# Performance work log

Measured on AMD Instinct MI355X. Metric: run time of the kernel, lower is better.

The kernel has to match this reference:

```python
import jax, jax.numpy as jnp
import numpy as np
from jax import lax

FEAT_STRIDE = 16
NMS_THRESH = 0.7
N_PRE = 6000   # test-mode n_test_pre_nms
N_POST = 300   # test-mode n_test_post_nms
MIN_SIZE = 16.0
SCALE = 1.0
RATIOS = (0.5, 1.0, 2.0)
ANCHOR_SCALES = (8, 16, 32)
BASE = 16
N_ANCHOR = len(RATIOS) * len(ANCHOR_SCALES)  # 9


def _anchor_base():
    py = px = BASE / 2.0
    ab = np.zeros((N_ANCHOR, 4), np.float32)
    for i, r in enumerate(RATIOS):
        for j, s in enumerate(ANCHOR_SCALES):
            h = BASE * s * np.sqrt(r)
            w = BASE * s * np.sqrt(1.0 / r)
            k = i * len(ANCHOR_SCALES) + j
            ab[k] = [py - h / 2.0, px - w / 2.0, py + h / 2.0, px + w / 2.0]
    return ab


def _anchors(hh, ww):
    # enumerate_shifted_anchor: (y1,x1,y2,x2) anchors for every feature cell
    ab = _anchor_base()
    sy = np.arange(0, hh * FEAT_STRIDE, FEAT_STRIDE)
    sx = np.arange(0, ww * FEAT_STRIDE, FEAT_STRIDE)
    SX, SY = np.meshgrid(sx, sy)
    shift = np.stack([SY.ravel(), SX.ravel(), SY.ravel(), SX.ravel()], 1)
    anc = (ab[None, :, :] + shift[:, None, :]).reshape(-1, 4).astype(np.float32)
    return jnp.asarray(anc)


def _iou(b):
    # b: [N,4] (y1,x1,y2,x2) -> [N,N] IoU
    y1, x1, y2, x2 = b[:, 0], b[:, 1], b[:, 2], b[:, 3]
    area = (y2 - y1) * (x2 - x1)
    ih = jnp.clip(jnp.minimum(y2[:, None], y2[None, :]) - jnp.maximum(y1[:, None], y1[None, :]), 0.0)
    iw = jnp.clip(jnp.minimum(x2[:, None], x2[None, :]) - jnp.maximum(x1[:, None], x1[None, :]), 0.0)
    inter = ih * iw
    return inter / (area[:, None] + area[None, :] - inter + 1e-9)


def _propose(loc, fg, anchor, img_h, img_w):
    # loc:[M,4] fg:[M] anchor:[M,4]  -> padded [N_POST,4] rois + valid mask
    ah = anchor[:, 2] - anchor[:, 0]
    aw = anchor[:, 3] - anchor[:, 1]
    acy = anchor[:, 0] + 0.5 * ah
    acx = anchor[:, 1] + 0.5 * aw
    cy = loc[:, 0] * ah + acy
    cx = loc[:, 1] * aw + acx
    h = jnp.exp(loc[:, 2]) * ah
    w = jnp.exp(loc[:, 3]) * aw
    roi = jnp.stack([
        jnp.clip(cy - 0.5 * h, 0.0, img_h),
        jnp.clip(cx - 0.5 * w, 0.0, img_w),
        jnp.clip(cy + 0.5 * h, 0.0, img_h),
        jnp.clip(cx + 0.5 * w, 0.0, img_w),
    ], axis=1)
    hs = roi[:, 2] - roi[:, 0]
    ws = roi[:, 3] - roi[:, 1]
    ms = MIN_SIZE * SCALE
    valid = (hs >= ms) & (ws >= ms)
    sc = jnp.where(valid, fg, -jnp.inf)  # drop too-small boxes from ranking
    top_sc, idx = lax.top_k(sc, N_PRE)   # score-sorted pre-NMS candidates
    boxes = roi[idx]
    ok = lax.stop_gradient(jnp.isfinite(top_sc))
    sup = lax.stop_gradient(_iou(boxes) > NMS_THRESH)  # [N_PRE,N_PRE]
    tri = jnp.arange(N_PRE)

    def body(i, keep):
        suppressed = jnp.any(keep & sup[:, i] & (tri < i))
        return keep.at[i].set(ok[i] & ~suppressed)

    keep = lax.fori_loop(0, N_PRE, body, jnp.zeros((N_PRE,), bool))
    rank = jnp.cumsum(keep.astype(jnp.int32)) - 1
    sel = keep & (rank < N_POST)
    tgt = jnp.where(sel, rank, N_POST)  # N_POST is out-of-bounds -> dropped
    out = jnp.zeros((N_POST, 4), boxes.dtype).at[tgt].set(boxes, mode='drop')
    vmask = jnp.zeros((N_POST,), bool).at[tgt].set(True, mode='drop')
    return out, vmask


def reference(x, conv1_w, conv1_b, score_w, score_b, loc_w, loc_b, img_h, img_w):
    n, _, hh, ww = x.shape
    anchor = _anchors(hh, ww)
    h = jax.nn.relu(
        lax.conv_general_dilated(x, conv1_w, (1, 1), 'SAME',
                                 dimension_numbers=('NCHW', 'OIHW', 'NCHW'))
        + conv1_b[None, :, None, None])
    locs = jnp.einsum('nchw,oc->nohw', h, loc_w[:, :, 0, 0]) + loc_b[None, :, None, None]
    scr = jnp.einsum('nchw,oc->nohw', h, score_w[:, :, 0, 0]) + score_b[None, :, None, None]
    rpn_locs = locs.transpose(0, 2, 3, 1).reshape(n, -1, 4)          # [n,M,4]
    scr_t = scr.transpose(0, 2, 3, 1)                                 # [n,hh,ww,2A]
    soft = jax.nn.softmax(scr_t.reshape(n, hh, ww, N_ANCHOR, 2), axis=-1)
    fg = soft[..., 1].reshape(n, -1)                                  # [n,M]
    rpn_scores = scr_t.reshape(n, -1, 2)
    rois, vmask = jax.vmap(lambda l, f: _propose(l, f, anchor, img_h, img_w))(rpn_locs, fg)
    roi_indices = jnp.broadcast_to(jnp.arange(n, dtype=jnp.int32)[:, None], (n, N_POST))
    return rpn_locs, rpn_scores, rois, roi_indices, anchor, vmask


def setup_inputs() -> dict:
    key = jax.random.key(0)
    ks = jax.random.split(key, 4)
    x = jax.random.normal(ks[0], (2, 512, 64, 64), jnp.float32)
    conv1_w = 0.01 * jax.random.normal(ks[1], (512, 512, 3, 3), jnp.float32)
    conv1_b = jnp.zeros((512,), jnp.float32)
    score_w = 0.01 * jax.random.normal(ks[2], (N_ANCHOR * 2, 512, 1, 1), jnp.float32)
    score_b = jnp.zeros((N_ANCHOR * 2,), jnp.float32)
    loc_w = 0.01 * jax.random.normal(ks[3], (N_ANCHOR * 4, 512, 1, 1), jnp.float32)
    loc_b = jnp.zeros((N_ANCHOR * 4,), jnp.float32)
    return {"x": x, "conv1_w": conv1_w, "conv1_b": conv1_b,
            "score_w": score_w, "score_b": score_b,
            "loc_w": loc_w, "loc_b": loc_b,
            "img_h": 1024, "img_w": 1024}
```

## Files before the change

kernel.cpp:

```cpp
#include <hip/hip_runtime.h>
#include <hip/hip_bf16.h>
#include <math.h>
#include <cstdint>

typedef unsigned long long u64;
typedef unsigned int u32;
typedef _Float16 half8 __attribute__((ext_vector_type(8)));
typedef float floatx4 __attribute__((ext_vector_type(4)));

#define NANCH 36864
#define SEG 65536
#define N_PRE 6000
#define N_POST 300
#define NW 96
#define NPADC 6144

#define O0 0
#define O1 294912
#define O2 442368
#define O3 444768
#define O4 445368
#define O5 592824

#define WS_XHI   0
#define WS_XLO   2097152
#define WS_WHI   4194304
#define WS_WLO   5373952
#define WS_WSLT  6553600
#define WS_WSLB  6586368
#define WS_H     6586432
#define WS_GUARD 10780736
#define WS_FG    0
#define WS_ROI   73728
#define WS_KEYS  368640
#define WS_SBOX  630784
#define WS_ALIVE 679936
#define WS_MASK  4194304

#define HSCALE 9.5367431640625e-07f

__device__ __forceinline__ void gl_lds16(const void* g, void* l) {
  __builtin_amdgcn_global_load_lds(
      (const __attribute__((address_space(1))) u32*)g,
      (__attribute__((address_space(3))) u32*)l, 16, 0, 0);
}

__device__ __forceinline__ u64 bcast64(u64 v, int src) {
  u32 lo = (u32)__shfl((int)(v & 0xFFFFFFFFull), src);
  u32 hi = (u32)__shfl((int)(v >> 32), src);
  return ((u64)hi << 32) | lo;
}

__global__ __launch_bounds__(256) void prep_all(
    const float* __restrict__ x, const float* __restrict__ w,
    const float* __restrict__ lw, const float* __restrict__ sw,
    const float* __restrict__ lb, const float* __restrict__ sb,
    float4* __restrict__ h, float4* __restrict__ guard,
    _Float16* __restrict__ xhi, _Float16* __restrict__ xlo,
    _Float16* __restrict__ whi, _Float16* __restrict__ wlo,
    float* __restrict__ wslt, float* __restrict__ wslb) {
  __shared__ float s[64 * 65];
  const int b = blockIdx.x, tid = threadIdx.x;
  if (b < 4097) {
    int idx = b * 256 + tid;
    if (idx < 1048576) h[idx] = make_float4(0.f, 0.f, 0.f, 0.f);
    else if (idx < 1048576 + 16) guard[idx - 1048576] = make_float4(0.f, 0.f, 0.f, 0.f);
    return;
  }
  if (b < 5121) {
    int l = b - 4097;
    int pt = l & 63, cg = (l >> 6) & 7, n = l >> 9;
    const int c0 = cg << 6, p0 = pt << 6;
#pragma unroll
    for (int kk = 0; kk < 16; ++kk) {
      int e = tid + (kk << 8);
      int ci = e >> 6, pi = e & 63;
      s[ci * 65 + pi] = x[(((size_t)(n * 512 + c0 + ci)) << 12) + p0 + pi];
    }
    __syncthreads();
#pragma unroll
    for (int kk = 0; kk < 16; ++kk) {
      int e = tid + (kk << 8);
      int ci = e & 63, pi = e >> 6;
      float sv = s[ci * 65 + pi] * 1024.f;
      _Float16 hi = (_Float16)sv;
      _Float16 lo = (_Float16)(sv - (float)hi);
      size_t off = (((size_t)(n << 12) + p0 + pi) << 9) + c0 + ci;
      xhi[off] = hi;
      xlo[off] = lo;
    }
    return;
  }
  if (b < 5697) {
    int l = b - 5121;
    int ct = l & 7, ot = (l >> 3) & 7, t = l >> 6;
    const int c0 = ct << 6, o0 = ot << 6;
#pragma unroll
    for (int kk = 0; kk < 16; ++kk) {
      int e = tid + (kk << 8);
      int ci = e & 63, oi = e >> 6;
      float sv = w[(size_t)(o0 + oi) * 4608 + (c0 + ci) * 9 + t] * 1024.f;
      _Float16 hi = (_Float16)sv;
      _Float16 lo = (_Float16)(sv - (float)hi);
      size_t off = ((size_t)((t << 9) + o0 + oi) << 9) + c0 + ci;
      whi[off] = hi;
      wlo[off] = lo;
    }
    return;
  }
  {
    int e = (b - 5697) * 256 + tid;
    if (e < 32768) {
      int c = e >> 6, o = e & 63;
      float v = 0.f;
      if (o < 36) v = lw[o * 512 + c];
      else if (o < 54) v = sw[(o - 36) * 512 + c];
      wslt[e] = v;
    } else if (e < 32832) {
      int o = e - 32768;
      float v = 0.f;
      if (o < 36) v = lb[o];
      else if (o < 54) v = sb[o - 36];
      wslb[o] = v;
    }
  }
}

__global__ __launch_bounds__(256) void conv_mfma(
    const _Float16* __restrict__ xhi, const _Float16* __restrict__ xlo,
    const _Float16* __restrict__ whi, const _Float16* __restrict__ wlo,
    const float* __restrict__ guard, float* __restrict__ hout) {
  __shared__ _Float16 aHi[4 * 68 * 32];
  __shared__ _Float16 aLo[4 * 68 * 32];
  __shared__ _Float16 bHi[128 * 32];
  __shared__ _Float16 bLo[128 * 32];
  const int tid = threadIdx.x;
  const int lane = tid & 63, w = tid >> 6;
  const int ptile = blockIdx.x;
  const int og = blockIdx.y;
  const int kq = blockIdx.z;
  const int n = ptile >> 5;
  const int y0 = (ptile & 31) << 1;
  const int o0 = og << 7;
  const int l15 = lane & 15, l16 = lane >> 4;
  const int ry = w >> 1;
  const int wo = (w & 1) << 6;

  floatx4 acc[4][4];
#pragma unroll
  for (int a = 0; a < 4; ++a)
#pragma unroll
    for (int b = 0; b < 4; ++b) acc[a][b] = (floatx4)0.f;

  for (int s = 0; s < 8; ++s) {
    const int c0 = (kq << 8) + (s << 5);
    __syncthreads();
    for (int i = w; i < 17; i += 4) {
      int chunk = (i << 6) + lane;
      int p = chunk >> 2, q = chunk & 3;
      int r = p / 68, xs = p - r * 68;
      int y = y0 - 1 + r, xg = xs - 1;
      bool ok = ((unsigned)y < 64u) && ((unsigned)xg < 64u);
      size_t off = (((size_t)(n << 12) + (y << 6) + xg) << 9) + c0 + (q << 3);
      const void* gh = ok ? (const void*)(xhi + off) : (const void*)guard;
      const void* gl = ok ? (const void*)(xlo + off) : (const void*)guard;
      gl_lds16(gh, (char*)aHi + (i << 10));
      gl_lds16(gl, (char*)aLo + (i << 10));
    }
    for (int tt = 0; tt < 9; ++tt) {
      if (tt > 0) __syncthreads();
      for (int i = w; i < 8; i += 4) {
        int chunk = (i << 6) + lane;
        int row = chunk >> 2, q = chunk & 3;
        size_t off = ((size_t)((tt << 9) + o0 + row) << 9) + c0 + (q << 3);
        gl_lds16((const void*)(whi + off), (char*)bHi + (i << 10));
        gl_lds16((const void*)(wlo + off), (char*)bLo + (i << 10));
      }
      __syncthreads();

      const int dy = tt / 3, dx = tt - 3 * dy;
      half8 ah[4], al[4], bh[4], bl[4];
#pragma unroll
      for (int im = 0; im < 4; ++im) {
        int xp = (im << 4) + l15;
        int p = (ry + dy) * 68 + xp + dx;
        ah[im] = *(const half8*)&aHi[(p << 5) + (l16 << 3)];
        al[im] = *(const half8*)&aLo[(p << 5) + (l16 << 3)];
      }
#pragma unroll
      for (int in = 0; in < 4; ++in) {
        int orow = wo + (in << 4) + l15;
        bh[in] = *(const half8*)&bHi[(orow << 5) + (l16 << 3)];
        bl[in] = *(const half8*)&bLo[(orow << 5) + (l16 << 3)];
      }
#pragma unroll
      for (int im = 0; im < 4; ++im)
#pragma unroll
        for (int in = 0; in < 4; ++in) {
          acc[im][in] = __builtin_amdgcn_mfma_f32_16x16x32_f16(
              ah[im], bh[in], acc[im][in], 0, 0, 0);
          acc[im][in] = __builtin_amdgcn_mfma_f32_16x16x32_f16(
              ah[im], bl[in], acc[im][in], 0, 0, 0);
          acc[im][in] = __builtin_amdgcn_mfma_f32_16x16x32_f16(
              al[im], bh[in], acc[im][in], 0, 0, 0);
        }
    }
  }

#pragma unroll
  for (int im = 0; im < 4; ++im)
#pragma unroll
    for (int in = 0; in < 4; ++in) {
      int o = o0 + wo + (in << 4) + l15;
#pragma unroll
      for (int reg = 0; reg < 4; ++reg) {
        int m_local = (ry << 6) + (im << 4) + (l16 << 2) + reg;
        size_t off = (((size_t)(n << 12) + (y0 << 6) + m_local) << 9) + o;
        atomicAdd(&hout[off], acc[im][in][reg]);
      }
    }
}

__global__ __launch_bounds__(256) void head_kernel(
    const float* __restrict__ hbuf, const float* __restrict__ cb,
    const float* __restrict__ wslt, const float* __restrict__ wslb,
    float* __restrict__ out, float* __restrict__ fgbuf) {
  const int y = blockIdx.x, n = blockIdx.y;
  __shared__ float sH[16 * 65];
  __shared__ float sWt[1024];
  __shared__ float sOut[64 * 65];
  const int tid = threadIdx.x;
  const int x = tid & 63, og = tid >> 6;

  float acc[16];
#pragma unroll
  for (int j = 0; j < 16; ++j) acc[j] = 0.f;

  const float* hb = hbuf + (((size_t)(n << 12) + (y << 6)) << 9);

  for (int c0 = 0; c0 < 512; c0 += 16) {
    __syncthreads();
#pragma unroll
    for (int p = 0; p < 4; ++p) {
      int e = tid + (p << 8);
      {
        int cc = e & 15, xx = e >> 4;
        float raw = hb[((size_t)xx << 9) + c0 + cc];
        sH[cc * 65 + xx] = fmaxf(raw * HSCALE + cb[c0 + cc], 0.f);
      }
      {
        int cc = e >> 6, xx = e & 63;
        sWt[e] = wslt[((c0 + cc) << 6) + xx];
      }
    }
    __syncthreads();
#pragma unroll
    for (int cc = 0; cc < 16; ++cc) {
      float hv = sH[cc * 65 + x];
      const float4* wp = (const float4*)&sWt[(cc << 6) + (og << 4)];
      float4 w0 = wp[0], w1 = wp[1], w2 = wp[2], w3 = wp[3];
      acc[0]  = fmaf(hv, w0.x, acc[0]);  acc[1]  = fmaf(hv, w0.y, acc[1]);
      acc[2]  = fmaf(hv, w0.z, acc[2]);  acc[3]  = fmaf(hv, w0.w, acc[3]);
      acc[4]  = fmaf(hv, w1.x, acc[4]);  acc[5]  = fmaf(hv, w1.y, acc[5]);
      acc[6]  = fmaf(hv, w1.z, acc[6]);  acc[7]  = fmaf(hv, w1.w, acc[7]);
      acc[8]  = fmaf(hv, w2.x, acc[8]);  acc[9]  = fmaf(hv, w2.y, acc[9]);
      acc[10] = fmaf(hv, w2.z, acc[10]); acc[11] = fmaf(hv, w2.w, acc[11]);
      acc[12] = fmaf(hv, w3.x, acc[12]); acc[13] = fmaf(hv, w3.y, acc[13]);
      acc[14] = fmaf(hv, w3.z, acc[14]); acc[15] = fmaf(hv, w3.w, acc[15]);
    }
  }
  __syncthreads();
#pragma unroll
  for (int j = 0; j < 16; ++j) {
    int o = (og << 4) + j;
    sOut[o * 65 + x] = acc[j] + wslb[o];
  }
  __syncthreads();

  const int p0 = (n << 12) + (y << 6);
  float* locs = out + O0 + (size_t)p0 * 36;
  for (int e = tid; e < 2304; e += 256) {
    int xx = e / 36, o = e - xx * 36;
    locs[e] = sOut[o * 65 + xx];
  }
  float* scrs = out + O1 + (size_t)p0 * 18;
  for (int e = tid; e < 1152; e += 256) {
    int xx = e / 18, ss = e - xx * 18;
    scrs[e] = sOut[(36 + ss) * 65 + xx];
  }
  float* fg = fgbuf + n * NANCH + (y << 6) * 9;
  for (int e = tid; e < 576; e += 256) {
    int xx = e / 9, a = e - xx * 9;
    float s0 = sOut[(36 + 2 * a) * 65 + xx];
    float s1 = sOut[(36 + 2 * a + 1) * 65 + xx];
    fg[e] = 1.0f / (1.0f + expf(s0 - s1));
  }
}

__global__ __launch_bounds__(256) void decode_kernel(
    const float* __restrict__ out0, const float* __restrict__ fgbuf,
    float4* __restrict__ roibuf, u64* __restrict__ keys,
    float* __restrict__ anchor_out, float* __restrict__ out,
    const int* __restrict__ imgh_p, const int* __restrict__ imgw_p) {
  int gid = blockIdx.x * 256 + threadIdx.x;
  if (gid < 3600) {
    if (gid < 2400) out[O2 + gid] = 0.f;
    else if (gid < 3000) out[O3 + (gid - 2400)] = (float)((gid - 2400) / 300);
    else out[O5 + (gid - 3000)] = 0.f;
  }
  int n = gid >> 16, k = gid & (SEG - 1);
  if (k >= NANCH) { keys[gid] = ~0ull; return; }
  int a = k % 9;
  int p = k / 9;
  int py = p >> 6, px = p & 63;

  const double R[3] = {0.5, 1.0, 2.0};
  const double S[3] = {8.0, 16.0, 32.0};
  double r = R[a / 3], s = S[a - (a / 3) * 3];
  double hd = 16.0 * s * sqrt(r);
  double wd = 16.0 * s * sqrt(1.0 / r);
  float ay1 = (float)(8.0 - hd / 2.0) + (float)(py * 16);
  float ax1 = (float)(8.0 - wd / 2.0) + (float)(px * 16);
  float ay2 = (float)(8.0 + hd / 2.0) + (float)(py * 16);
  float ax2 = (float)(8.0 + wd / 2.0) + (float)(px * 16);
  if (n == 0) {
    float* ao = anchor_out + (size_t)k * 4;
    ao[0] = ay1; ao[1] = ax1; ao[2] = ay2; ao[3] = ax2;
  }
  float ahk = ay2 - ay1, awk = ax2 - ax1;
  float acy = ay1 + 0.5f * ahk, acx = ax1 + 0.5f * awk;
  const float* lp = out0 + ((size_t)(n * NANCH + k) << 2);
  float dy = lp[0], dx = lp[1], dh = lp[2], dw = lp[3];
  float cy = dy * ahk + acy;
  float cx = dx * awk + acx;
  float bh = expf(dh) * ahk;
  float bw = expf(dw) * awk;
  float img_h = (float)imgh_p[0], img_w = (float)imgw_p[0];
  float y1 = fminf(fmaxf(cy - 0.5f * bh, 0.f), img_h);
  float x1 = fminf(fmaxf(cx - 0.5f * bw, 0.f), img_w);
  float y2 = fminf(fmaxf(cy + 0.5f * bh, 0.f), img_h);
  float x2 = fminf(fmaxf(cx + 0.5f * bw, 0.f), img_w);
  bool valid = ((y2 - y1) >= 16.f) && ((x2 - x1) >= 16.f);
  float sc = valid ? fgbuf[n * NANCH + k] : -INFINITY;
  roibuf[n * NANCH + k] = make_float4(y1, x1, y2, x2);
  unsigned int b = __float_as_uint(sc);
  unsigned int m = b ^ ((b & 0x80000000u) ? 0xFFFFFFFFu : 0x80000000u);
  keys[gid] = ((u64)(~m) << 32) | (unsigned int)k;
}

__global__ __launch_bounds__(256) void sort_local_a(u64* __restrict__ keys) {
  __shared__ u64 sk[4096];
  const int base = blockIdx.x << 12;
  for (int e = threadIdx.x; e < 4096; e += 256) sk[e] = keys[base + e];
  __syncthreads();
  for (int k = 2; k <= 4096; k <<= 1) {
    for (int j = k >> 1; j > 0; j >>= 1) {
      for (int t = threadIdx.x; t < 2048; t += 256) {
        int l = ((t & ~(j - 1)) << 1) | (t & (j - 1));
        int rr = l | j;
        bool asc = (((base + l) & k) == 0);
        u64 a = sk[l], b = sk[rr];
        if ((a > b) == asc) { sk[l] = b; sk[rr] = a; }
      }
      __syncthreads();
    }
  }
  for (int e = threadIdx.x; e < 4096; e += 256) keys[base + e] = sk[e];
}

__global__ __launch_bounds__(256) void sort_global_pass(u64* __restrict__ keys,
                                                        int k, int j) {
  int t = blockIdx.x * 256 + threadIdx.x;
  int l = ((t & ~(j - 1)) << 1) | (t & (j - 1));
  int rr = l | j;
  bool asc = (((l & (SEG - 1)) & k) == 0);
  u64 a = keys[l], b = keys[rr];
  if ((a > b) == asc) { keys[l] = b; keys[rr] = a; }
}

__global__ __launch_bounds__(256) void sort_global_pass2(u64* __restrict__ keys,
                                                         int k, int j1) {
  int t = blockIdx.x * 256 + threadIdx.x;
  int j2 = j1 >> 1;
  int l = ((t & ~(j2 - 1)) << 1) | (t & (j2 - 1));
  l = ((l & ~(j1 - 1)) << 1) | (l & (j1 - 1));
  u64 e0 = keys[l], e1 = keys[l | j2], e2 = keys[l | j1], e3 = keys[l | j1 | j2];
  bool asc = (((l & (SEG - 1)) & k) == 0);
  u64 tmp;
  if ((e0 > e2) == asc) { tmp = e0; e0 = e2; e2 = tmp; }
  if ((e1 > e3) == asc) { tmp = e1; e1 = e3; e3 = tmp; }
  if ((e0 > e1) == asc) { tmp = e0; e0 = e1; e1 = tmp; }
  if ((e2 > e3) == asc) { tmp = e2; e2 = e3; e3 = tmp; }
  keys[l] = e0; keys[l | j2] = e1; keys[l | j1] = e2; keys[l | j1 | j2] = e3;
}

__global__ __launch_bounds__(256) void sort_local_b(u64* __restrict__ keys, int k) {
  __shared__ u64 sk[4096];
  const int base = blockIdx.x << 12;
  for (int e = threadIdx.x; e < 4096; e += 256) sk[e] = keys[base + e];
  __syncthreads();
  for (int j = 2048; j > 0; j >>= 1) {
    for (int t = threadIdx.x; t < 2048; t += 256) {
      int l = ((t & ~(j - 1)) << 1) | (t & (j - 1));
      int rr = l | j;
      bool asc = ((((base + l) & (SEG - 1)) & k) == 0);
      u64 a = sk[l], b = sk[rr];
      if ((a > b) == asc) { sk[l] = b; sk[rr] = a; }
    }
    __syncthreads();
  }
  for (int e = threadIdx.x; e < 4096; e += 256) keys[base + e] = sk[e];
}

__global__ __launch_bounds__(256) void nms_gather(
    const u64* __restrict__ keys, const float4* __restrict__ roibuf,
    float4* __restrict__ sbox, u64* __restrict__ alive) {
  const int n = blockIdx.y;
  int i = blockIdx.x * 256 + threadIdx.x;
  u64 kk = (i < N_PRE) ? keys[(n << 16) + i] : ~0ull;
  bool valid = ((unsigned)(kk >> 32)) < 0xFF800000u;
  float4 b = make_float4(0.f, 0.f, 0.f, 0.f);
  if (valid) b = roibuf[(size_t)n * NANCH + (unsigned)(kk & 0xFFFFFFFFull)];
  sbox[n * NPADC + i] = b;
  u64 bal = __ballot(valid);
  if ((threadIdx.x & 63) == 0) alive[n * NW + (i >> 6)] = bal;
}

__global__ __launch_bounds__(256) void build_mask(
    const float4* __restrict__ sbox, u64* __restrict__ M) {
  __shared__ float4 jb[4][64];
  __shared__ float ja[4][64];
  const int tid = threadIdx.x, lane = tid & 63, wv = tid >> 6;
  const int g = blockIdx.x, q = blockIdx.y, n = blockIdx.z;
  const float4* sb = sbox + n * NPADC;
  float4 bi = sb[(g << 6) + lane];
  float ai = (bi.z - bi.x) * (bi.w - bi.y);
  u64* Mrow = M + ((size_t)(n * NPADC + (g << 6) + lane)) * NW;
#pragma unroll
  for (int it = 0; it < 6; ++it) {
    int w = q * 24 + (it << 2) + wv;
    float4 bjl = sb[(w << 6) + lane];
    jb[wv][lane] = bjl;
    ja[wv][lane] = (bjl.z - bjl.x) * (bjl.w - bjl.y);
    u64 bits = 0;
#pragma unroll 8
    for (int j = 0; j < 64; ++j) {
      float4 bj = jb[wv][j];
      float aj = ja[wv][j];
      float ih = fmaxf(fminf(bi.z, bj.z) - fmaxf(bi.x, bj.x), 0.f);
      float iw = fmaxf(fminf(bi.w, bj.w) - fmaxf(bi.y, bj.y), 0.f);
      float inter = ih * iw;
      bool bit = inter / (ai + aj - inter + 1e-9f) > 0.7f;
      bits |= ((u64)bit) << j;
    }
    Mrow[w] = bits;
  }
}

__global__ __launch_bounds__(64) void nms_reduce(
    const u64* __restrict__ M, const u64* __restrict__ alive,
    const float4* __restrict__ sbox, float* __restrict__ out) {
  const int n = blockIdx.x, lane = threadIdx.x;
  float* rois = out + O2 + n * (N_POST * 4);
  float* vmask = out + O5 + n * N_POST;
  const u64* A = alive + n * NW;
  const u64* Mb = M + (size_t)n * NPADC * NW;
  const float4* sb = sbox + n * NPADC;
  u64 aw0 = A[lane];
  u64 aw1 = (lane < 32) ? A[64 + lane] : 0ull;
  u64 accA = 0, accB = 0;
  int nk = 0;
  u64 dnext = Mb[(size_t)lane * NW + 0];
  float4 bnext = sb[lane];
  const u64 below = lane ? (~0ull >> (64 - lane)) : 0ull;

  for (int c = 0; c < 94; ++c) {
    u64 dcur = dnext;
    float4 bcur = bnext;
    if (c + 1 < 94) {
      dnext = Mb[(size_t)(((c + 1) << 6) + lane) * NW + (c + 1)];
      bnext = sb[((c + 1) << 6) + lane];
    }
    u64 wacc = (c < 64) ? bcast64(accA, c) : bcast64(accB, c - 64);
    u64 aw = (c < 64) ? bcast64(aw0, c) : bcast64(aw1, c - 64);
    u64 alive_u = aw & ~wacc;
    if (alive_u == 0ull) continue;

    u64 dmask = dcur & below;
    u64 rem = alive_u, kept = 0;
    while (rem) {
      int j = __builtin_ctzll(rem);
      kept |= 1ull << j;
      u64 col = __ballot((dmask >> j) & 1);
      rem &= ~(col | (1ull << j));
    }

    int npop = __popcll(kept);
    if ((kept >> lane) & 1ull) {
      int slot = nk + __popcll(kept & below);
      if (slot < N_POST) {
        rois[slot * 4 + 0] = bcur.x; rois[slot * 4 + 1] = bcur.y;
        rois[slot * 4 + 2] = bcur.z; rois[slot * 4 + 3] = bcur.w;
        vmask[slot] = 1.0f;
      }
    }
    if (nk + npop >= N_POST) break;
    nk += npop;

    u64 kk = kept;
    while (kk) {
      int j0 = __builtin_ctzll(kk); kk &= kk - 1;
      int j1 = kk ? __builtin_ctzll(kk) : j0; kk &= kk - 1;
      int j2 = kk ? __builtin_ctzll(kk) : j0; kk &= kk - 1;
      int j3 = kk ? __builtin_ctzll(kk) : j0; kk &= kk - 1;
      int j4 = kk ? __builtin_ctzll(kk) : j0; kk &= kk - 1;
      int j5 = kk ? __builtin_ctzll(kk) : j0; kk &= kk - 1;
      int j6 = kk ? __builtin_ctzll(kk) : j0; kk &= kk - 1;
      int j7 = kk ? __builtin_ctzll(kk) : j0; kk &= kk - 1;
      const u64* r0 = Mb + (size_t)((c << 6) + j0) * NW;
      const u64* r1 = Mb + (size_t)((c << 6) + j1) * NW;
      const u64* r2 = Mb + (size_t)((c << 6) + j2) * NW;
      const u64* r3 = Mb + (size_t)((c << 6) + j3) * NW;
      const u64* r4 = Mb + (size_t)((c << 6) + j4) * NW;
      const u64* r5 = Mb + (size_t)((c << 6) + j5) * NW;
      const u64* r6 = Mb + (size_t)((c << 6) + j6) * NW;
      const u64* r7 = Mb + (size_t)((c << 6) + j7) * NW;
      u64 oA = r0[lane] | r1[lane] | r2[lane] | r3[lane]
             | r4[lane] | r5[lane] | r6[lane] | r7[lane];
      u64 oB = 0;
      if (lane < 32)
        oB = r0[64 + lane] | r1[64 + lane] | r2[64 + lane] | r3[64 + lane]
           | r4[64 + lane] | r5[64 + lane] | r6[64 + lane] | r7[64 + lane];
      accA |= oA;
      accB |= oB;
    }
  }
}

extern "C" void kernel_launch(void* const* d_in, const int* in_sizes, int n_in,
                              void* d_out, int out_size, void* d_ws, size_t ws_size,
                              hipStream_t stream) {
  const float* x        = (const float*)d_in[0];
  const float* conv1_w  = (const float*)d_in[1];
  const float* conv1_b  = (const float*)d_in[2];
  const float* score_w  = (const float*)d_in[3];
  const float* score_b  = (const float*)d_in[4];
  const float* loc_w    = (const float*)d_in[5];
  const float* loc_b    = (const float*)d_in[6];
  const int*   imgh_p   = (const int*)d_in[7];
  const int*   imgw_p   = (const int*)d_in[8];

  float* out = (float*)d_out;
  float* ws  = (float*)d_ws;

  _Float16* xhi = (_Float16*)(ws + WS_XHI);
  _Float16* xlo = (_Float16*)(ws + WS_XLO);
  _Float16* whi = (_Float16*)(ws + WS_WHI);
  _Float16* wlo = (_Float16*)(ws + WS_WLO);
  float* wslt   = ws + WS_WSLT;
  float* wslb   = ws + WS_WSLB;
  float* hbuf   = ws + WS_H;
  float* guard  = ws + WS_GUARD;
  float* fgbuf   = ws + WS_FG;
  float4* roibuf = (float4*)(ws + WS_ROI);
  u64* keys      = (u64*)(ws + WS_KEYS);
  float4* sbox   = (float4*)(ws + WS_SBOX);
  u64* alive     = (u64*)(ws + WS_ALIVE);
  u64* maskbuf   = (u64*)(ws + WS_MASK);

  prep_all<<<5826, 256, 0, stream>>>(x, conv1_w, loc_w, score_w, loc_b, score_b,
                                     (float4*)hbuf, (float4*)guard,
                                     xhi, xlo, whi, wlo, wslt, wslb);

  conv_mfma<<<dim3(64, 4, 2), 256, 0, stream>>>(xhi, xlo, whi, wlo, guard, hbuf);

  head_kernel<<<dim3(64, 2), 256, 0, stream>>>(hbuf, conv1_b, wslt, wslb, out, fgbuf);
  decode_kernel<<<512, 256, 0, stream>>>(out, fgbuf, roibuf, keys,
                                         out + O4, out, imgh_p, imgw_p);

  sort_local_a<<<32, 256, 0, stream>>>(keys);
  for (int k = 8192; k <= SEG; k <<= 1) {
    int j = k >> 1;
    while (j >= 4096) {
      if (j >= 8192) {
        sort_global_pass2<<<128, 256, 0, stream>>>(keys, k, j);
        j >>= 2;
      } else {
        sort_global_pass<<<256, 256, 0, stream>>>(keys, k, j);
        j >>= 1;
      }
    }
    sort_local_b<<<32, 256, 0, stream>>>(keys, k);
  }

  nms_gather<<<dim3(24, 2), 256, 0, stream>>>(keys, roibuf, sbox, alive);
  build_mask<<<dim3(96, 4, 2), 256, 0, stream>>>(sbox, maskbuf);
  nms_reduce<<<2, 64, 0, stream>>>(maskbuf, alive, sbox, out);
}
```

Baseline: 501.1 us.

## Double-buffer weight tiles in conv MFMA loop with vmcnt-based prefetch

The conv kernel now keeps two LDS buffers for the weight tiles and issues the next tap's weight loads before computing the current one. Explicit s_waitcnt vmcnt plus raw s_barrier replace the syncthreads pairs, so weight fetch latency can overlap with the MFMA work. It also raises wave priority around the MFMA block. The A-tile reload at a new channel slice is issued without its own wait, so ordering relies on the vmcnt counting being correct. LDS use grows by 16KB.

Result: no change. 505.9 us (+1.0%).

```diff
diff --git a/kernel.cpp b/kernel.cpp
--- a/kernel.cpp
+++ b/kernel.cpp
@@ -38,6 +38,8 @@
 #define WS_MASK  4194304
 
 #define HSCALE 9.5367431640625e-07f
+
+#define WAITVM(N) asm volatile("s_waitcnt vmcnt(" #N ")" ::: "memory")
 
 __device__ __forceinline__ void gl_lds16(const void* g, void* l) {
   __builtin_amdgcn_global_load_lds(
@@ -132,8 +134,8 @@
     const float* __restrict__ guard, float* __restrict__ hout) {
   __shared__ _Float16 aHi[4 * 68 * 32];
   __shared__ _Float16 aLo[4 * 68 * 32];
-  __shared__ _Float16 bHi[128 * 32];
-  __shared__ _Float16 bLo[128 * 32];
+  __shared__ _Float16 bHi[2][128 * 32];
+  __shared__ _Float16 bLo[2][128 * 32];
   const int tid = threadIdx.x;
   const int lane = tid & 63, w = tid >> 6;
   const int ptile = blockIdx.x;
@@ -152,9 +154,8 @@
 #pragma unroll
     for (int b = 0; b < 4; ++b) acc[a][b] = (floatx4)0.f;
 
-  for (int s = 0; s < 8; ++s) {
+  auto stage_a = [&](int s) {
     const int c0 = (kq << 8) + (s << 5);
-    __syncthreads();
     for (int i = w; i < 17; i += 4) {
       int chunk = (i << 6) + lane;
       int p = chunk >> 2, q = chunk & 3;
@@ -167,16 +168,36 @@
       gl_lds16(gh, (char*)aHi + (i << 10));
       gl_lds16(gl, (char*)aLo + (i << 10));
     }
+  };
+  auto stage_b = [&](int s, int tt, int bb) {
+    const int c0 = (kq << 8) + (s << 5);
+    for (int i = w; i < 8; i += 4) {
+      int chunk = (i << 6) + lane;
+      int row = chunk >> 2, q = chunk & 3;
+      size_t off = ((size_t)((tt << 9) + o0 + row) << 9) + c0 + (q << 3);
+      gl_lds16((const void*)(whi + off), (char*)&bHi[bb][0] + (i << 10));
+      gl_lds16((const void*)(wlo + off), (char*)&bLo[bb][0] + (i << 10));
+    }
+  };
+
+  stage_a(0);
+  stage_b(0, 0, 0);
+  int buf = 0;
+
+  for (int s = 0; s < 8; ++s) {
+    if (s > 0) stage_a(s);
     for (int tt = 0; tt < 9; ++tt) {
-      if (tt > 0) __syncthreads();
-      for (int i = w; i < 8; i += 4) {
-        int chunk = (i << 6) + lane;
-        int row = chunk >> 2, q = chunk & 3;
-        size_t off = ((size_t)((tt << 9) + o0 + row) << 9) + c0 + (q << 3);
-        gl_lds16((const void*)(whi + off), (char*)bHi + (i << 10));
-        gl_lds16((const void*)(wlo + off), (char*)bLo + (i << 10));
-      }
-      __syncthreads();
+      const bool lastIter = (s == 7) && (tt == 8);
+      if (!lastIter) {
+        const int ns = (tt == 8) ? s + 1 : s;
+        const int ntt = (tt == 8) ? 0 : tt + 1;
+        stage_b(ns, ntt, buf ^ 1);
+        WAITVM(4);
+      } else {
+        WAITVM(0);
+      }
+      __builtin_amdgcn_s_barrier();
+      asm volatile("" ::: "memory");
 
       const int dy = tt / 3, dx = tt - 3 * dy;
       half8 ah[4], al[4], bh[4], bl[4];
@@ -190,9 +211,10 @@
 #pragma unroll
       for (int in = 0; in < 4; ++in) {
         int orow = wo + (in << 4) + l15;
-        bh[in] = *(const half8*)&bHi[(orow << 5) + (l16 << 3)];
-        bl[in] = *(const half8*)&bLo[(orow << 5) + (l16 << 3)];
-      }
+        bh[in] = *(const half8*)&bHi[buf][(orow << 5) + (l16 << 3)];
+        bl[in] = *(const half8*)&bLo[buf][(orow << 5) + (l16 << 3)];
+      }
+      __builtin_amdgcn_s_setprio(1);
 #pragma unroll
       for (int im = 0; im < 4; ++im)
 #pragma unroll
@@ -204,6 +226,10 @@
           acc[im][in] = __builtin_amdgcn_mfma_f32_16x16x32_f16(
               al[im], bh[in], acc[im][in], 0, 0, 0);
         }
+      __builtin_amdgcn_s_setprio(0);
+      asm volatile("" ::: "memory");
+      __builtin_amdgcn_s_barrier();
+      buf ^= 1;
     }
   }
 
```

## Split conv split-fp16 product terms across grid z instead of channel halves

Applied to the files above, without the earlier changes.

The 3x3 conv previously split the 512 input channels into two halves along grid z. Each block loaded both hi and lo fp16 parts of activations and weights and issued three MFMAs per tile. Now each of three z-blocks handles one product term (hi*hi, hi*lo, lo*hi) over all 512 channels, loading only one A and one B buffer. This halves LDS use and per-block register pressure, and raises block count from 512 to 768, at the cost of re-reading activations and weights more times from global memory and doing more atomic adds to the output.

New measurement: 590.3 us. 1.18x slower.

```diff
diff --git a/kernel.cpp b/kernel.cpp
--- a/kernel.cpp
+++ b/kernel.cpp
@@ -130,15 +130,15 @@
     const _Float16* __restrict__ xhi, const _Float16* __restrict__ xlo,
     const _Float16* __restrict__ whi, const _Float16* __restrict__ wlo,
     const float* __restrict__ guard, float* __restrict__ hout) {
-  __shared__ _Float16 aHi[4 * 68 * 32];
-  __shared__ _Float16 aLo[4 * 68 * 32];
-  __shared__ _Float16 bHi[128 * 32];
-  __shared__ _Float16 bLo[128 * 32];
+  __shared__ _Float16 aS[4 * 68 * 32];
+  __shared__ _Float16 bS[128 * 32];
   const int tid = threadIdx.x;
   const int lane = tid & 63, w = tid >> 6;
   const int ptile = blockIdx.x;
   const int og = blockIdx.y;
-  const int kq = blockIdx.z;
+  const int pass = blockIdx.z;
+  const _Float16* __restrict__ Asrc = (pass == 2) ? xlo : xhi;
+  const _Float16* __restrict__ Bsrc = (pass == 1) ? wlo : whi;
   const int n = ptile >> 5;
   const int y0 = (ptile & 31) << 1;
   const int o0 = og << 7;
@@ -152,8 +152,8 @@
 #pragma unroll
     for (int b = 0; b < 4; ++b) acc[a][b] = (floatx4)0.f;
 
-  for (int s = 0; s < 8; ++s) {
-    const int c0 = (kq << 8) + (s << 5);
+  for (int s = 0; s < 16; ++s) {
+    const int c0 = s << 5;
     __syncthreads();
     for (int i = w; i < 17; i += 4) {
       int chunk = (i << 6) + lane;
@@ -162,10 +162,8 @@
       int y = y0 - 1 + r, xg = xs - 1;
       bool ok = ((unsigned)y < 64u) && ((unsigned)xg < 64u);
       size_t off = (((size_t)(n << 12) + (y << 6) + xg) << 9) + c0 + (q << 3);
-      const void* gh = ok ? (const void*)(xhi + off) : (const void*)guard;
-      const void* gl = ok ? (const void*)(xlo + off) : (const void*)guard;
-      gl_lds16(gh, (char*)aHi + (i << 10));
-      gl_lds16(gl, (char*)aLo + (i << 10));
+      const void* ga = ok ? (const void*)(Asrc + off) : (const void*)guard;
+      gl_lds16(ga, (char*)aS + (i << 10));
     }
     for (int tt = 0; tt < 9; ++tt) {
       if (tt > 0) __syncthreads();
@@ -173,37 +171,29 @@
         int chunk = (i << 6) + lane;
         int row = chunk >> 2, q = chunk & 3;
         size_t off = ((size_t)((tt << 9) + o0 + row) << 9) + c0 + (q << 3);
-        gl_lds16((const void*)(whi + off), (char*)bHi + (i << 10));
-        gl_lds16((const void*)(wlo + off), (char*)bLo + (i << 10));
+        gl_lds16((const void*)(Bsrc + off), (char*)bS + (i << 10));
       }
       __syncthreads();
 
       const int dy = tt / 3, dx = tt - 3 * dy;
-      half8 ah[4], al[4], bh[4], bl[4];
+      half8 av[4], bv[4];
 #pragma unroll
       for (int im = 0; im < 4; ++im) {
         int xp = (im << 4) + l15;
         int p = (ry + dy) * 68 + xp + dx;
-        ah[im] = *(const half8*)&aHi[(p << 5) + (l16 << 3)];
-        al[im] = *(const half8*)&aLo[(p << 5) + (l16 << 3)];
+        av[im] = *(const half8*)&aS[(p << 5) + (l16 << 3)];
       }
 #pragma unroll
       for (int in = 0; in < 4; ++in) {
         int orow = wo + (in << 4) + l15;
-        bh[in] = *(const half8*)&bHi[(orow << 5) + (l16 << 3)];
-        bl[in] = *(const half8*)&bLo[(orow << 5) + (l16 << 3)];
+        bv[in] = *(const half8*)&bS[(orow << 5) + (l16 << 3)];
       }
 #pragma unroll
       for (int im = 0; im < 4; ++im)
 #pragma unroll
-        for (int in = 0; in < 4; ++in) {
+        for (int in = 0; in < 4; ++in)
           acc[im][in] = __builtin_amdgcn_mfma_f32_16x16x32_f16(
-              ah[im], bh[in], acc[im][in], 0, 0, 0);
-          acc[im][in] = __builtin_amdgcn_mfma_f32_16x16x32_f16(
-              ah[im], bl[in], acc[im][in], 0, 0, 0);
-          acc[im][in] = __builtin_amdgcn_mfma_f32_16x16x32_f16(
-              al[im], bh[in], acc[im][in], 0, 0, 0);
-        }
+              av[im], bv[in], acc[im][in], 0, 0, 0);
     }
   }
 
@@ -572,7 +562,7 @@
                                      (float4*)hbuf, (float4*)guard,
                                      xhi, xlo, whi, wlo, wslt, wslb);
 
-  conv_mfma<<<dim3(64, 4, 2), 256, 0, stream>>>(xhi, xlo, whi, wlo, guard, hbuf);
+  conv_mfma<<<dim3(64, 4, 3), 256, 0, stream>>>(xhi, xlo, whi, wlo, guard, hbuf);
 
   head_kernel<<<dim3(64, 2), 256, 0, stream>>>(hbuf, conv1_b, wslt, wslb, out, fgbuf);
   decode_kernel<<<512, 256, 0, stream>>>(out, fgbuf, roibuf, keys,
```

## Load conv weights directly to registers with double-buffered prefetch, drop LDS staging

Applied to the files above, without the earlier changes.

The weight (B) tiles in the MFMA conv kernel used to be staged through shared memory, with two barriers per 3x3 tap. Each lane now loads its own B fragments straight from global memory into registers. The next tap's fragments are prefetched while the current tap's MFMAs run. This removes the per-tap barriers and the B LDS traffic, but raises register pressure from the double-buffered half8 arrays and issues uncoalesced per-lane 16-byte global loads.

New measurement: 544.0 us. +8.6%, slower.

```diff
diff --git a/kernel.cpp b/kernel.cpp
--- a/kernel.cpp
+++ b/kernel.cpp
@@ -132,8 +132,6 @@
     const float* __restrict__ guard, float* __restrict__ hout) {
   __shared__ _Float16 aHi[4 * 68 * 32];
   __shared__ _Float16 aLo[4 * 68 * 32];
-  __shared__ _Float16 bHi[128 * 32];
-  __shared__ _Float16 bLo[128 * 32];
   const int tid = threadIdx.x;
   const int lane = tid & 63, w = tid >> 6;
   const int ptile = blockIdx.x;
@@ -151,6 +149,10 @@
   for (int a = 0; a < 4; ++a)
 #pragma unroll
     for (int b = 0; b < 4; ++b) acc[a][b] = (floatx4)0.f;
+
+  const size_t bbase = ((size_t)(o0 + wo + l15) << 9) + (l16 << 3);
+
+  half8 bh[2][4], bl[2][4];
 
   for (int s = 0; s < 8; ++s) {
     const int c0 = (kq << 8) + (s << 5);
@@ -167,42 +169,48 @@
       gl_lds16(gh, (char*)aHi + (i << 10));
       gl_lds16(gl, (char*)aLo + (i << 10));
     }
+    {
+      const size_t base0 = bbase + c0;
+#pragma unroll
+      for (int in = 0; in < 4; ++in) {
+        size_t off = base0 + ((size_t)in << 13);
+        bh[0][in] = *(const half8*)(whi + off);
+        bl[0][in] = *(const half8*)(wlo + off);
+      }
+    }
+    __syncthreads();
+
+#pragma unroll
     for (int tt = 0; tt < 9; ++tt) {
-      if (tt > 0) __syncthreads();
-      for (int i = w; i < 8; i += 4) {
-        int chunk = (i << 6) + lane;
-        int row = chunk >> 2, q = chunk & 3;
-        size_t off = ((size_t)((tt << 9) + o0 + row) << 9) + c0 + (q << 3);
-        gl_lds16((const void*)(whi + off), (char*)bHi + (i << 10));
-        gl_lds16((const void*)(wlo + off), (char*)bLo + (i << 10));
-      }
-      __syncthreads();
-
+      const int cur = tt & 1, nxt = (tt + 1) & 1;
+      if (tt < 8) {
+        const size_t basen = ((size_t)(tt + 1) << 18) + bbase + c0;
+#pragma unroll
+        for (int in = 0; in < 4; ++in) {
+          size_t off = basen + ((size_t)in << 13);
+          bh[nxt][in] = *(const half8*)(whi + off);
+          bl[nxt][in] = *(const half8*)(wlo + off);
+        }
+      }
       const int dy = tt / 3, dx = tt - 3 * dy;
-      half8 ah[4], al[4], bh[4], bl[4];
+      half8 av[4], alv[4];
 #pragma unroll
       for (int im = 0; im < 4; ++im) {
         int xp = (im << 4) + l15;
         int p = (ry + dy) * 68 + xp + dx;
-        ah[im] = *(const half8*)&aHi[(p << 5) + (l16 << 3)];
-        al[im] = *(const half8*)&aLo[(p << 5) + (l16 << 3)];
-      }
-#pragma unroll
-      for (int in = 0; in < 4; ++in) {
-        int orow = wo + (in << 4) + l15;
-        bh[in] = *(const half8*)&bHi[(orow << 5) + (l16 << 3)];
-        bl[in] = *(const half8*)&bLo[(orow << 5) + (l16 << 3)];
+        av[im] = *(const half8*)&aHi[(p << 5) + (l16 << 3)];
+        alv[im] = *(const half8*)&aLo[(p << 5) + (l16 << 3)];
       }
 #pragma unroll
       for (int im = 0; im < 4; ++im)
 #pragma unroll
         for (int in = 0; in < 4; ++in) {
           acc[im][in] = __builtin_amdgcn_mfma_f32_16x16x32_f16(
-              ah[im], bh[in], acc[im][in], 0, 0, 0);
+              av[im], bh[cur][in], acc[im][in], 0, 0, 0);
           acc[im][in] = __builtin_amdgcn_mfma_f32_16x16x32_f16(
-              ah[im], bl[in], acc[im][in], 0, 0, 0);
+              av[im], bl[cur][in], acc[im][in], 0, 0, 0);
           acc[im][in] = __builtin_amdgcn_mfma_f32_16x16x32_f16(
-              al[im], bh[in], acc[im][in], 0, 0, 0);
+              alv[im], bh[cur][in], acc[im][in], 0, 0, 0);
         }
     }
   }
```
